# Kernel optimization log

Measured on AMD Instinct MI355X. Metric: run time of the kernel, lower is better.

## Reference

```python
import jax, jax.numpy as jnp
import numpy as np

N = 50000      # nodes
E = 800000     # edges
INS = 128
H = 128
OUTS = 128
G = 512        # graphs in batch
BN_EPS = 1e-5


def _lin(k, fan_in, fan_out):
    s = 1.0 / np.sqrt(fan_in)
    kw, kb = jax.random.split(k)
    w = jax.random.uniform(kw, (fan_in, fan_out), minval=-s, maxval=s, dtype=jnp.float32)
    b = jax.random.uniform(kb, (fan_out,), minval=-s, maxval=s, dtype=jnp.float32)
    return w, b


def setup_inputs() -> dict:
    key = jax.random.key(0)
    ks = jax.random.split(key, 16)
    x = jax.random.normal(ks[0], (N, INS), dtype=jnp.float32)
    edge_src = jax.random.randint(ks[1], (E,), 0, N, dtype=jnp.int32)
    edge_dst = jax.random.randint(ks[2], (E,), 0, N, dtype=jnp.int32)
    ptr = jnp.sort(jax.random.randint(ks[3], (G + 1,), 0, N, dtype=jnp.int32))
    ptr = ptr.at[0].set(0).at[-1].set(N)
    w1a, b1a = _lin(ks[4], INS, H)
    w1b, b1b = _lin(ks[5], H, H)
    w2a, b2a = _lin(ks[6], H, H)
    w2b, b2b = _lin(ks[7], H, H)
    w3a, b3a = _lin(ks[8], H, H)
    w3b, b3b = _lin(ks[9], H, OUTS)
    g1 = jnp.ones((H,), jnp.float32); be1 = jnp.zeros((H,), jnp.float32)
    g2 = jnp.ones((H,), jnp.float32); be2 = jnp.zeros((H,), jnp.float32)
    g3 = jnp.ones((H,), jnp.float32); be3 = jnp.zeros((H,), jnp.float32)
    return dict(x=x, edge_src=edge_src, edge_dst=edge_dst, ptr=ptr,
                w1a=w1a, b1a=b1a, g1=g1, be1=be1, w1b=w1b, b1b=b1b,
                w2a=w2a, b2a=b2a, g2=g2, be2=be2, w2b=w2b, b2b=b2b,
                w3a=w3a, b3a=b3a, g3=g3, be3=be3, w3b=w3b, b3b=b3b)


def _bn(h, gamma, beta):
    # BatchNorm1d in training mode: stats over the node dimension
    mu = jnp.mean(h, axis=0)
    var = jnp.var(h, axis=0)
    return gamma * (h - mu) * jax.lax.rsqrt(var + BN_EPS) + beta


def _gin_layer(h, src, dst, wa, ba, gamma, beta, wb, bb):
    # GINConv (eps=0): mlp(x + sum_{j in N(i)} x_j)
    agg = jax.ops.segment_sum(h[src], dst, num_segments=N)  # [N, d]
    h = h + agg
    h = jax.nn.relu(_bn(h @ wa + ba, gamma, beta))
    h = jax.nn.relu(h @ wb + bb)
    return h


def reference(x, edge_src, edge_dst, ptr,
              w1a, b1a, g1, be1, w1b, b1b,
              w2a, b2a, g2, be2, w2b, b2b,
              w3a, b3a, g3, be3, w3b, b3b):
    h = _gin_layer(x, edge_src, edge_dst, w1a, b1a, g1, be1, w1b, b1b)
    h = _gin_layer(h, edge_src, edge_dst, w2a, b2a, g2, be2, w2b, b2b)
    h = _gin_layer(h, edge_src, edge_dst, w3a, b3a, g3, be3, w3b, b3b)
    # segment_csr(x, ptr, reduce='sum') readout
    seg = jnp.searchsorted(ptr, jnp.arange(N, dtype=jnp.int32), side='right') - 1
    return jax.ops.segment_sum(h, seg, num_segments=G)  # [G, OUTS]
```

## Files before the change

kernel.cpp:

```cpp
#include <hip/hip_runtime.h>

#define NNODES 50000
#define NEDGES 800000
#define HD 128
#define NG 512
#define BN_EPS 1e-5f
#define NTILE 3125
#define NSPLIT 32

typedef short bf16x8 __attribute__((ext_vector_type(8)));
typedef float floatx4 __attribute__((ext_vector_type(4)));

union U16 { uint4 u; bf16x8 h; };

__device__ __forceinline__ ushort f2bf(float f) {
    unsigned u = __float_as_uint(f);
    return (ushort)((u + 0x7fffu + ((u >> 16) & 1u)) >> 16);
}
__device__ __forceinline__ void unpack8(const uint4& u, float* f) {
    const unsigned* w = (const unsigned*)&u;
#pragma unroll
    for (int i = 0; i < 4; ++i) {
        f[2 * i]     = __uint_as_float(w[i] << 16);
        f[2 * i + 1] = __uint_as_float(w[i] & 0xffff0000u);
    }
}
__device__ __forceinline__ uint4 pack8(const float* f) {
    uint4 o;
    unsigned* w = (unsigned*)&o;
#pragma unroll
    for (int i = 0; i < 4; ++i)
        w[i] = (unsigned)f2bf(f[2 * i]) | ((unsigned)f2bf(f[2 * i + 1]) << 16);
    return o;
}


__global__ void hist_kernel(const int* __restrict__ dst, int* __restrict__ cnt, int n) {
    int i = blockIdx.x * 256 + threadIdx.x;
    if (i < n) atomicAdd(&cnt[dst[i]], 1);
}

__global__ void scan1_kernel(const int* __restrict__ cnt, int* __restrict__ incl,
                             int* __restrict__ bsum, int n) {
    __shared__ int s[1024];
    int i = blockIdx.x * 1024 + threadIdx.x;
    int v = (i < n) ? cnt[i] : 0;
    s[threadIdx.x] = v;
    __syncthreads();
    for (int off = 1; off < 1024; off <<= 1) {
        int add = (threadIdx.x >= off) ? s[threadIdx.x - off] : 0;
        __syncthreads();
        s[threadIdx.x] += add;
        __syncthreads();
    }
    if (i < n) incl[i] = s[threadIdx.x];
    if (threadIdx.x == 1023) bsum[blockIdx.x] = s[1023];
}

__global__ void scan2_kernel(const int* __restrict__ bsum, int* __restrict__ boffs, int nb) {
    __shared__ int s[64];
    int v = (threadIdx.x < nb) ? bsum[threadIdx.x] : 0;
    s[threadIdx.x] = v;
    __syncthreads();
    for (int off = 1; off < 64; off <<= 1) {
        int add = (threadIdx.x >= off) ? s[threadIdx.x - off] : 0;
        __syncthreads();
        s[threadIdx.x] += add;
        __syncthreads();
    }
    if (threadIdx.x < nb) boffs[threadIdx.x] = s[threadIdx.x] - v;
}

__global__ void scan3_kernel(const int* __restrict__ incl, const int* __restrict__ boffs,
                             int* __restrict__ rowp, int n) {
    int i = blockIdx.x * 256 + threadIdx.x;
    if (i < n) rowp[i + 1] = incl[i] + boffs[i >> 10];
    if (i == 0) rowp[0] = 0;
}

__global__ void build_kernel(const int* __restrict__ src, const int* __restrict__ dst,
                             const int* __restrict__ rowp, int* __restrict__ fill,
                             int* __restrict__ colv, int n) {
    int i = blockIdx.x * 256 + threadIdx.x;
    if (i < n) {
        int d = dst[i];
        int pos = rowp[d] + atomicAdd(&fill[d], 1);
        colv[pos] = src[i];
    }
}


__global__ void cvt_kernel(const float* __restrict__ x, ushort* __restrict__ xb, int n4) {
    int i = blockIdx.x * 256 + threadIdx.x;
    if (i < n4) {
        float4 v = ((const float4*)x)[i];
        ushort4 o;
        o.x = f2bf(v.x); o.y = f2bf(v.y); o.z = f2bf(v.z); o.w = f2bf(v.w);
        ((ushort4*)xb)[i] = o;
    }
}


struct WP6 { const float* w[6]; };

__global__ void wfrag_kernel(WP6 p, ushort* __restrict__ wf) {
    const float* W = p.w[blockIdx.x];
    ushort* o = wf + (size_t)blockIdx.x * 16384;
    for (int i = threadIdx.x; i < 16384; i += 256) {
        int j = i & 7, lane = (i >> 3) & 63, kc = (i >> 9) & 3, ct = i >> 11;
        int k = kc * 32 + (lane >> 4) * 8 + j;
        int n = ct * 16 + (lane & 15);
        o[i] = f2bf(W[k * HD + n]);
    }
}


__global__ __launch_bounds__(256) void aggregate_kernel(
    const ushort* __restrict__ h, const int* __restrict__ rowp,
    const int* __restrict__ colv, ushort* __restrict__ outv, int n) {
    int node = blockIdx.x * 16 + (threadIdx.x >> 4);
    int l = threadIdx.x & 15;
    if (node >= n) return;
    int beg = rowp[node], end = rowp[node + 1];
    const uint4* hp = (const uint4*)h;
    float a[8];
    uint4 sv = hp[(size_t)node * 16 + l];
    unpack8(sv, a);
    for (int j = beg; j < end; ++j) {
        uint4 v = hp[(size_t)colv[j] * 16 + l];
        float b[8];
        unpack8(v, b);
#pragma unroll
        for (int i = 0; i < 8; ++i) a[i] += b[i];
    }
    ((uint4*)outv)[(size_t)node * 16 + l] = pack8(a);
}


template <bool STATS, bool PRE_BN, bool READOUT>
__global__ __launch_bounds__(256, 4) void mfma_gemm_kernel(
    const ushort* __restrict__ A, const ushort* __restrict__ Wf,
    const float* __restrict__ bias, ushort* __restrict__ out,
    const float* __restrict__ sca, const float* __restrict__ shf,
    float* __restrict__ ssum_p, float* __restrict__ ssq_p,
    const int* __restrict__ gptr, float* __restrict__ gout) {
    __shared__ ushort cbuf[16 * HD];
    __shared__ float reds[HD];
    __shared__ float redq[HD];
    const int t = threadIdx.x;
    const int wave = t >> 6, lane = t & 63;
    const int quad = lane >> 4, l16 = lane & 15;
    const int row0 = blockIdx.x * 16;
    const int rowA = row0 + l16;

    const uint4* Wf4 = (const uint4*)Wf;
    uint4 bfr[2][4];
#pragma unroll
    for (int c = 0; c < 2; ++c)
#pragma unroll
        for (int kc = 0; kc < 4; ++kc)
            bfr[c][kc] = Wf4[((2 * wave + c) * 4 + kc) * 64 + lane];

    U16 afr[4];
    {
        const ushort* ap = A + (size_t)rowA * HD + quad * 8;
#pragma unroll
        for (int kc = 0; kc < 4; ++kc)
            afr[kc].u = *(const uint4*)(ap + kc * 32);
    }
    if (PRE_BN) {
#pragma unroll
        for (int kc = 0; kc < 4; ++kc) {
            float f[8];
            unpack8(afr[kc].u, f);
            int kb = kc * 32 + quad * 8;
            float4 s0 = ((const float4*)(sca + kb))[0];
            float4 s1 = ((const float4*)(sca + kb))[1];
            float4 h0 = ((const float4*)(shf + kb))[0];
            float4 h1 = ((const float4*)(shf + kb))[1];
            f[0] = fmaxf(fmaf(f[0], s0.x, h0.x), 0.f);
            f[1] = fmaxf(fmaf(f[1], s0.y, h0.y), 0.f);
            f[2] = fmaxf(fmaf(f[2], s0.z, h0.z), 0.f);
            f[3] = fmaxf(fmaf(f[3], s0.w, h0.w), 0.f);
            f[4] = fmaxf(fmaf(f[4], s1.x, h1.x), 0.f);
            f[5] = fmaxf(fmaf(f[5], s1.y, h1.y), 0.f);
            f[6] = fmaxf(fmaf(f[6], s1.z, h1.z), 0.f);
            f[7] = fmaxf(fmaf(f[7], s1.w, h1.w), 0.f);
            afr[kc].u = pack8(f);
        }
    }

    floatx4 zf = {0.f, 0.f, 0.f, 0.f};
    floatx4 acc[2] = {zf, zf};
#pragma unroll
    for (int kc = 0; kc < 4; ++kc) {
#pragma unroll
        for (int c = 0; c < 2; ++c) {
            U16 bu;
            bu.u = bfr[c][kc];
            acc[c] = __builtin_amdgcn_mfma_f32_16x16x32_bf16(afr[kc].h, bu.h, acc[c], 0, 0, 0);
        }
    }

    if (READOUT) {
        int r_base = row0 + quad * 4;
        int lo = 0, hi = NG - 1;
        while (lo < hi) {
            int mid = (lo + hi) >> 1;
            if (r_base >= gptr[mid + 1]) lo = mid + 1; else hi = mid;
        }
        int segr[4];
        int sg = lo;
#pragma unroll
        for (int reg = 0; reg < 4; ++reg) {
            while (r_base + reg >= gptr[sg + 1]) ++sg;
            segr[reg] = sg;
        }
#pragma unroll
        for (int c = 0; c < 2; ++c) {
            int col = (2 * wave + c) * 16 + l16;
            float b = bias[col];
            float run = 0.f;
            int cur = segr[0];
#pragma unroll
            for (int reg = 0; reg < 4; ++reg) {
                if (segr[reg] != cur) {
                    if (run != 0.f) atomicAdd(&gout[cur * HD + col], run);
                    run = 0.f;
                    cur = segr[reg];
                }
                run += fmaxf(acc[c][reg] + b, 0.f);
            }
            if (run != 0.f) atomicAdd(&gout[cur * HD + col], run);
        }
        return;
    }

    const int lrow = quad * 4;
#pragma unroll
    for (int c = 0; c < 2; ++c) {
        int col = (2 * wave + c) * 16 + l16;
        float b = bias[col];
        float s = 0.f, q = 0.f;
#pragma unroll
        for (int reg = 0; reg < 4; ++reg) {
            float v = acc[c][reg] + b;
            if (!STATS) v = fmaxf(v, 0.f);
            cbuf[(lrow + reg) * HD + col] = f2bf(v);
            if (STATS) { s += v; q += v * v; }
        }
        if (STATS) {
            s += __shfl_xor(s, 16); s += __shfl_xor(s, 32);
            q += __shfl_xor(q, 16); q += __shfl_xor(q, 32);
            if (quad == 0) { reds[col] = s; redq[col] = q; }
        }
    }
    __syncthreads();

    {
        const uint4* c4 = (const uint4*)cbuf;
        uint4* o4 = (uint4*)out;
        int row = t >> 4, part = t & 15;
        o4[(size_t)(row0 + row) * 16 + part] = c4[t];
    }

    if (STATS) {
        int slot = (blockIdx.x & (NSPLIT - 1)) * HD;
        if (t < HD) atomicAdd(&ssum_p[slot + t], reds[t]);
        else        atomicAdd(&ssq_p[slot + (t - HD)], redq[t - HD]);
    }
}

__global__ void finalize_stats_kernel(const float* __restrict__ sp, const float* __restrict__ qp,
                                      const float* __restrict__ gamma, const float* __restrict__ beta,
                                      float* __restrict__ sca, float* __restrict__ shf) {
    int c = threadIdx.x;
    float s = 0.f, q = 0.f;
#pragma unroll
    for (int i = 0; i < NSPLIT; ++i) { s += sp[i * HD + c]; q += qp[i * HD + c]; }
    float mean = s / (float)NNODES;
    float var = q / (float)NNODES - mean * mean;
    float rstd = rsqrtf(var + BN_EPS);
    float sc = gamma[c] * rstd;
    sca[c] = sc;
    shf[c] = beta[c] - mean * sc;
}


extern "C" void kernel_launch(void* const* d_in, const int* in_sizes, int n_in,
                              void* d_out, int out_size, void* d_ws, size_t ws_size,
                              hipStream_t stream) {
    const float* x = (const float*)d_in[0];
    const int* esrc = (const int*)d_in[1];
    const int* edst = (const int*)d_in[2];
    const int* gptr = (const int*)d_in[3];
    const float* wA[3] = {(const float*)d_in[4], (const float*)d_in[10], (const float*)d_in[16]};
    const float* bA[3] = {(const float*)d_in[5], (const float*)d_in[11], (const float*)d_in[17]};
    const float* gm[3] = {(const float*)d_in[6], (const float*)d_in[12], (const float*)d_in[18]};
    const float* bt[3] = {(const float*)d_in[7], (const float*)d_in[13], (const float*)d_in[19]};
    const float* wB[3] = {(const float*)d_in[8], (const float*)d_in[14], (const float*)d_in[20]};
    const float* bB[3] = {(const float*)d_in[9], (const float*)d_in[15], (const float*)d_in[21]};

    char* w = (char*)d_ws;
    ushort* xb   = (ushort*)w; w += (size_t)NNODES * HD * 2;
    ushort* tmpb = (ushort*)w; w += (size_t)NNODES * HD * 2;
    ushort* zbb  = (ushort*)w; w += (size_t)NNODES * HD * 2;
    ushort* hbb  = (ushort*)w; w += (size_t)NNODES * HD * 2;
    ushort* wf   = (ushort*)w; w += (size_t)6 * 16384 * 2;
    int* colv  = (int*)w;   w += (size_t)NEDGES * 4;
    int* incl  = (int*)w;   w += (size_t)NNODES * 4;
    int* rowp  = (int*)w;   w += ((size_t)(NNODES + 1) * 4 + 15) & ~(size_t)15;
    int* bsum  = (int*)w;   w += 64 * 4;
    int* boffs = (int*)w;   w += 64 * 4;
    float* scab = (float*)w; w += 3 * 128 * 4;
    float* shfb = (float*)w; w += 3 * 128 * 4;
    char* zero_base = w;
    int* cnt   = (int*)w;   w += (size_t)NNODES * 4;
    int* fill  = (int*)w;   w += (size_t)NNODES * 4;
    float* ssum_p = (float*)w; w += 3 * NSPLIT * 128 * 4;
    float* ssq_p  = (float*)w; w += 3 * NSPLIT * 128 * 4;
    size_t zero_bytes = (size_t)(w - zero_base);

    hipMemsetAsync(zero_base, 0, zero_bytes, stream);
    hipMemsetAsync(d_out, 0, (size_t)NG * HD * 4, stream);

    hist_kernel<<<(NEDGES + 255) / 256, 256, 0, stream>>>(edst, cnt, NEDGES);
    int nsb = (NNODES + 1023) / 1024;
    scan1_kernel<<<nsb, 1024, 0, stream>>>(cnt, incl, bsum, NNODES);
    scan2_kernel<<<1, 64, 0, stream>>>(bsum, boffs, nsb);
    scan3_kernel<<<(NNODES + 255) / 256, 256, 0, stream>>>(incl, boffs, rowp, NNODES);
    build_kernel<<<(NEDGES + 255) / 256, 256, 0, stream>>>(esrc, edst, rowp, fill, colv, NEDGES);

    cvt_kernel<<<(NNODES * HD / 4 + 255) / 256, 256, 0, stream>>>(x, xb, NNODES * HD / 4);
    WP6 wp;
    wp.w[0] = wA[0]; wp.w[1] = wB[0]; wp.w[2] = wA[1];
    wp.w[3] = wB[1]; wp.w[4] = wA[2]; wp.w[5] = wB[2];
    wfrag_kernel<<<6, 256, 0, stream>>>(wp, wf);

    const int agg_grid = (NNODES + 15) / 16;
    const ushort* hin = xb;
    for (int l = 0; l < 3; ++l) {
        aggregate_kernel<<<agg_grid, 256, 0, stream>>>(hin, rowp, colv, tmpb, NNODES);
        mfma_gemm_kernel<true, false, false><<<NTILE, 256, 0, stream>>>(
            tmpb, wf + (size_t)(2 * l) * 16384, bA[l], zbb, nullptr, nullptr,
            ssum_p + l * NSPLIT * 128, ssq_p + l * NSPLIT * 128, nullptr, nullptr);
        finalize_stats_kernel<<<1, 128, 0, stream>>>(
            ssum_p + l * NSPLIT * 128, ssq_p + l * NSPLIT * 128,
            gm[l], bt[l], scab + l * 128, shfb + l * 128);
        if (l < 2) {
            mfma_gemm_kernel<false, true, false><<<NTILE, 256, 0, stream>>>(
                zbb, wf + (size_t)(2 * l + 1) * 16384, bB[l], hbb,
                scab + l * 128, shfb + l * 128, nullptr, nullptr, nullptr, nullptr);
        } else {
            mfma_gemm_kernel<false, true, true><<<NTILE, 256, 0, stream>>>(
                zbb, wf + (size_t)(2 * l + 1) * 16384, bB[l], nullptr,
                scab + l * 128, shfb + l * 128, nullptr, nullptr,
                gptr, (float*)d_out);
        }
        hin = hbb;
    }
}
```

Baseline: 458.4 us.

## Fuse aggregation into first GEMM, fold BN finalize into second GEMM, merge prep kernels

The neighbor-sum aggregation now runs inside the first GEMM kernel and stages its result in shared memory, so the bf16 intermediate buffer is no longer written and read back. The BatchNorm stats finalize moves into every block of the second GEMM, and the stat-slot count drops from 32 to 8. Histogram, input conversion and weight fragment packing merge into one prep kernel, and the scan's second and third passes merge into one. This cuts kernel launches and global memory traffic. The cost is more atomic contention on fewer stat slots, redundant finalize work in each block, and aggregation load imbalance now sitting inside the GEMM blocks.

New measurement: 422.0 us. 7.9% less time.

```diff
diff --git a/kernel.cpp b/kernel.cpp
--- a/kernel.cpp
+++ b/kernel.cpp
@@ -6,7 +6,9 @@
 #define NG 512
 #define BN_EPS 1e-5f
 #define NTILE 3125
-#define NSPLIT 32
+#define NSPLIT 8
+#define NSB 49
+#define AROW 136
 
 typedef short bf16x8 __attribute__((ext_vector_type(8)));
 typedef float floatx4 __attribute__((ext_vector_type(4)));
@@ -35,10 +37,34 @@
 }
 
 
-__global__ void hist_kernel(const int* __restrict__ dst, int* __restrict__ cnt, int n) {
-    int i = blockIdx.x * 256 + threadIdx.x;
-    if (i < n) atomicAdd(&cnt[dst[i]], 1);
-}
+struct WP6 { const float* w[6]; };
+
+__global__ __launch_bounds__(256) void prep_kernel(
+    const int* __restrict__ edst, int* __restrict__ cnt,
+    const float* __restrict__ x, ushort* __restrict__ xb,
+    WP6 p, ushort* __restrict__ wf) {
+    const int b = blockIdx.x, t = threadIdx.x;
+    if (b < 3125) {
+        atomicAdd(&cnt[edst[b * 256 + t]], 1);
+    } else if (b < 9375) {
+        int i = (b - 3125) * 256 + t;
+        float4 v = ((const float4*)x)[i];
+        ushort4 o;
+        o.x = f2bf(v.x); o.y = f2bf(v.y); o.z = f2bf(v.z); o.w = f2bf(v.w);
+        ((ushort4*)xb)[i] = o;
+    } else {
+        int m = b - 9375;
+        const float* W = p.w[m];
+        ushort* o = wf + (size_t)m * 16384;
+        for (int i = t; i < 16384; i += 256) {
+            int j = i & 7, lane = (i >> 3) & 63, kc = (i >> 9) & 3, ct = i >> 11;
+            int k = kc * 32 + (lane >> 4) * 8 + j;
+            int n = ct * 16 + (lane & 15);
+            o[i] = f2bf(W[k * HD + n]);
+        }
+    }
+}
+
 
 __global__ void scan1_kernel(const int* __restrict__ cnt, int* __restrict__ incl,
                              int* __restrict__ bsum, int n) {
@@ -57,24 +83,22 @@
     if (threadIdx.x == 1023) bsum[blockIdx.x] = s[1023];
 }
 
-__global__ void scan2_kernel(const int* __restrict__ bsum, int* __restrict__ boffs, int nb) {
-    __shared__ int s[64];
-    int v = (threadIdx.x < nb) ? bsum[threadIdx.x] : 0;
-    s[threadIdx.x] = v;
-    __syncthreads();
-    for (int off = 1; off < 64; off <<= 1) {
-        int add = (threadIdx.x >= off) ? s[threadIdx.x - off] : 0;
-        __syncthreads();
-        s[threadIdx.x] += add;
-        __syncthreads();
-    }
-    if (threadIdx.x < nb) boffs[threadIdx.x] = s[threadIdx.x] - v;
-}
-
-__global__ void scan3_kernel(const int* __restrict__ incl, const int* __restrict__ boffs,
-                             int* __restrict__ rowp, int n) {
-    int i = blockIdx.x * 256 + threadIdx.x;
-    if (i < n) rowp[i + 1] = incl[i] + boffs[i >> 10];
+__global__ void scan23_kernel(const int* __restrict__ incl, const int* __restrict__ bsum,
+                              int* __restrict__ rowp, int n) {
+    __shared__ int bpre[64];
+    const int t = threadIdx.x;
+    if (t < 64) {
+        int own = (t < NSB) ? bsum[t] : 0;
+        int v = own;
+        for (int off = 1; off < 64; off <<= 1) {
+            int u = __shfl_up(v, off);
+            if (t >= off) v += u;
+        }
+        bpre[t] = v - own;
+    }
+    __syncthreads();
+    int i = blockIdx.x * 256 + t;
+    if (i < n) rowp[i + 1] = incl[i] + bpre[i >> 10];
     if (i == 0) rowp[0] = 0;
 }
 
@@ -90,60 +114,12 @@
 }
 
 
-__global__ void cvt_kernel(const float* __restrict__ x, ushort* __restrict__ xb, int n4) {
-    int i = blockIdx.x * 256 + threadIdx.x;
-    if (i < n4) {
-        float4 v = ((const float4*)x)[i];
-        ushort4 o;
-        o.x = f2bf(v.x); o.y = f2bf(v.y); o.z = f2bf(v.z); o.w = f2bf(v.w);
-        ((ushort4*)xb)[i] = o;
-    }
-}
-
-
-struct WP6 { const float* w[6]; };
-
-__global__ void wfrag_kernel(WP6 p, ushort* __restrict__ wf) {
-    const float* W = p.w[blockIdx.x];
-    ushort* o = wf + (size_t)blockIdx.x * 16384;
-    for (int i = threadIdx.x; i < 16384; i += 256) {
-        int j = i & 7, lane = (i >> 3) & 63, kc = (i >> 9) & 3, ct = i >> 11;
-        int k = kc * 32 + (lane >> 4) * 8 + j;
-        int n = ct * 16 + (lane & 15);
-        o[i] = f2bf(W[k * HD + n]);
-    }
-}
-
-
-__global__ __launch_bounds__(256) void aggregate_kernel(
-    const ushort* __restrict__ h, const int* __restrict__ rowp,
-    const int* __restrict__ colv, ushort* __restrict__ outv, int n) {
-    int node = blockIdx.x * 16 + (threadIdx.x >> 4);
-    int l = threadIdx.x & 15;
-    if (node >= n) return;
-    int beg = rowp[node], end = rowp[node + 1];
-    const uint4* hp = (const uint4*)h;
-    float a[8];
-    uint4 sv = hp[(size_t)node * 16 + l];
-    unpack8(sv, a);
-    for (int j = beg; j < end; ++j) {
-        uint4 v = hp[(size_t)colv[j] * 16 + l];
-        float b[8];
-        unpack8(v, b);
-#pragma unroll
-        for (int i = 0; i < 8; ++i) a[i] += b[i];
-    }
-    ((uint4*)outv)[(size_t)node * 16 + l] = pack8(a);
-}
-
-
-template <bool STATS, bool PRE_BN, bool READOUT>
-__global__ __launch_bounds__(256, 4) void mfma_gemm_kernel(
-    const ushort* __restrict__ A, const ushort* __restrict__ Wf,
+__global__ __launch_bounds__(256, 4) void gemmA_kernel(
+    const ushort* __restrict__ H, const int* __restrict__ rowp,
+    const int* __restrict__ colv, const ushort* __restrict__ Wf,
     const float* __restrict__ bias, ushort* __restrict__ out,
-    const float* __restrict__ sca, const float* __restrict__ shf,
-    float* __restrict__ ssum_p, float* __restrict__ ssq_p,
-    const int* __restrict__ gptr, float* __restrict__ gout) {
+    float* __restrict__ ssum_p, float* __restrict__ ssq_p) {
+    __shared__ ushort abuf[16 * AROW];
     __shared__ ushort cbuf[16 * HD];
     __shared__ float reds[HD];
     __shared__ float redq[HD];
@@ -151,6 +127,95 @@
     const int wave = t >> 6, lane = t & 63;
     const int quad = lane >> 4, l16 = lane & 15;
     const int row0 = blockIdx.x * 16;
+
+    const uint4* Wf4 = (const uint4*)Wf;
+    uint4 bfr[2][4];
+#pragma unroll
+    for (int c = 0; c < 2; ++c)
+#pragma unroll
+        for (int kc = 0; kc < 4; ++kc)
+            bfr[c][kc] = Wf4[((2 * wave + c) * 4 + kc) * 64 + lane];
+
+    {
+        int nl = t >> 4;
+        int node = row0 + nl;
+        int l = t & 15;
+        int beg = rowp[node], end = rowp[node + 1];
+        const uint4* hp = (const uint4*)H;
+        float a[8];
+        unpack8(hp[(size_t)node * 16 + l], a);
+        for (int j = beg; j < end; ++j) {
+            float b[8];
+            unpack8(hp[(size_t)colv[j] * 16 + l], b);
+#pragma unroll
+            for (int i = 0; i < 8; ++i) a[i] += b[i];
+        }
+        *(uint4*)&abuf[nl * AROW + l * 8] = pack8(a);
+    }
+    __syncthreads();
+
+    U16 afr[4];
+#pragma unroll
+    for (int kc = 0; kc < 4; ++kc)
+        afr[kc].u = *(const uint4*)&abuf[l16 * AROW + kc * 32 + quad * 8];
+
+    floatx4 zf = {0.f, 0.f, 0.f, 0.f};
+    floatx4 acc[2] = {zf, zf};
+#pragma unroll
+    for (int kc = 0; kc < 4; ++kc) {
+#pragma unroll
+        for (int c = 0; c < 2; ++c) {
+            U16 bu;
+            bu.u = bfr[c][kc];
+            acc[c] = __builtin_amdgcn_mfma_f32_16x16x32_bf16(afr[kc].h, bu.h, acc[c], 0, 0, 0);
+        }
+    }
+
+    const int lrow = quad * 4;
+#pragma unroll
+    for (int c = 0; c < 2; ++c) {
+        int col = (2 * wave + c) * 16 + l16;
+        float b = bias[col];
+        float s = 0.f, q = 0.f;
+#pragma unroll
+        for (int reg = 0; reg < 4; ++reg) {
+            float v = acc[c][reg] + b;
+            cbuf[(lrow + reg) * HD + col] = f2bf(v);
+            s += v; q += v * v;
+        }
+        s += __shfl_xor(s, 16); s += __shfl_xor(s, 32);
+        q += __shfl_xor(q, 16); q += __shfl_xor(q, 32);
+        if (quad == 0) { reds[col] = s; redq[col] = q; }
+    }
+    __syncthreads();
+
+    {
+        const uint4* c4 = (const uint4*)cbuf;
+        uint4* o4 = (uint4*)out;
+        int row = t >> 4, part = t & 15;
+        o4[(size_t)(row0 + row) * 16 + part] = c4[t];
+    }
+
+    int slot = (blockIdx.x & (NSPLIT - 1)) * HD;
+    if (t < HD) atomicAdd(&ssum_p[slot + t], reds[t]);
+    else        atomicAdd(&ssq_p[slot + (t - HD)], redq[t - HD]);
+}
+
+
+template <bool READOUT>
+__global__ __launch_bounds__(256, 4) void gemmB_kernel(
+    const ushort* __restrict__ A, const ushort* __restrict__ Wf,
+    const float* __restrict__ bias, ushort* __restrict__ out,
+    const float* __restrict__ gamma, const float* __restrict__ beta,
+    const float* __restrict__ ssum_p, const float* __restrict__ ssq_p,
+    const int* __restrict__ gptr, float* __restrict__ gout) {
+    __shared__ ushort cbuf[16 * HD];
+    __shared__ float sca[HD];
+    __shared__ float shf[HD];
+    const int t = threadIdx.x;
+    const int wave = t >> 6, lane = t & 63;
+    const int quad = lane >> 4, l16 = lane & 15;
+    const int row0 = blockIdx.x * 16;
     const int rowA = row0 + l16;
 
     const uint4* Wf4 = (const uint4*)Wf;
@@ -168,26 +233,38 @@
         for (int kc = 0; kc < 4; ++kc)
             afr[kc].u = *(const uint4*)(ap + kc * 32);
     }
-    if (PRE_BN) {
-#pragma unroll
-        for (int kc = 0; kc < 4; ++kc) {
-            float f[8];
-            unpack8(afr[kc].u, f);
-            int kb = kc * 32 + quad * 8;
-            float4 s0 = ((const float4*)(sca + kb))[0];
-            float4 s1 = ((const float4*)(sca + kb))[1];
-            float4 h0 = ((const float4*)(shf + kb))[0];
-            float4 h1 = ((const float4*)(shf + kb))[1];
-            f[0] = fmaxf(fmaf(f[0], s0.x, h0.x), 0.f);
-            f[1] = fmaxf(fmaf(f[1], s0.y, h0.y), 0.f);
-            f[2] = fmaxf(fmaf(f[2], s0.z, h0.z), 0.f);
-            f[3] = fmaxf(fmaf(f[3], s0.w, h0.w), 0.f);
-            f[4] = fmaxf(fmaf(f[4], s1.x, h1.x), 0.f);
-            f[5] = fmaxf(fmaf(f[5], s1.y, h1.y), 0.f);
-            f[6] = fmaxf(fmaf(f[6], s1.z, h1.z), 0.f);
-            f[7] = fmaxf(fmaf(f[7], s1.w, h1.w), 0.f);
-            afr[kc].u = pack8(f);
-        }
+
+    if (t < HD) {
+        float s = 0.f, q = 0.f;
+#pragma unroll
+        for (int i = 0; i < NSPLIT; ++i) { s += ssum_p[i * HD + t]; q += ssq_p[i * HD + t]; }
+        float mean = s / (float)NNODES;
+        float var = q / (float)NNODES - mean * mean;
+        float rstd = rsqrtf(var + BN_EPS);
+        float sc = gamma[t] * rstd;
+        sca[t] = sc;
+        shf[t] = beta[t] - mean * sc;
+    }
+    __syncthreads();
+
+#pragma unroll
+    for (int kc = 0; kc < 4; ++kc) {
+        float f[8];
+        unpack8(afr[kc].u, f);
+        int kb = kc * 32 + quad * 8;
+        float4 s0 = ((const float4*)(sca + kb))[0];
+        float4 s1 = ((const float4*)(sca + kb))[1];
+        float4 h0 = ((const float4*)(shf + kb))[0];
+        float4 h1 = ((const float4*)(shf + kb))[1];
+        f[0] = fmaxf(fmaf(f[0], s0.x, h0.x), 0.f);
+        f[1] = fmaxf(fmaf(f[1], s0.y, h0.y), 0.f);
+        f[2] = fmaxf(fmaf(f[2], s0.z, h0.z), 0.f);
+        f[3] = fmaxf(fmaf(f[3], s0.w, h0.w), 0.f);
+        f[4] = fmaxf(fmaf(f[4], s1.x, h1.x), 0.f);
+        f[5] = fmaxf(fmaf(f[5], s1.y, h1.y), 0.f);
+        f[6] = fmaxf(fmaf(f[6], s1.z, h1.z), 0.f);
+        f[7] = fmaxf(fmaf(f[7], s1.w, h1.w), 0.f);
+        afr[kc].u = pack8(f);
     }
 
     floatx4 zf = {0.f, 0.f, 0.f, 0.f};
@@ -241,49 +318,17 @@
     for (int c = 0; c < 2; ++c) {
         int col = (2 * wave + c) * 16 + l16;
         float b = bias[col];
-        float s = 0.f, q = 0.f;
-#pragma unroll
-        for (int reg = 0; reg < 4; ++reg) {
-            float v = acc[c][reg] + b;
-            if (!STATS) v = fmaxf(v, 0.f);
-            cbuf[(lrow + reg) * HD + col] = f2bf(v);
-            if (STATS) { s += v; q += v * v; }
-        }
-        if (STATS) {
-            s += __shfl_xor(s, 16); s += __shfl_xor(s, 32);
-            q += __shfl_xor(q, 16); q += __shfl_xor(q, 32);
-            if (quad == 0) { reds[col] = s; redq[col] = q; }
-        }
-    }
-    __syncthreads();
-
+#pragma unroll
+        for (int reg = 0; reg < 4; ++reg)
+            cbuf[(lrow + reg) * HD + col] = f2bf(fmaxf(acc[c][reg] + b, 0.f));
+    }
+    __syncthreads();
     {
         const uint4* c4 = (const uint4*)cbuf;
         uint4* o4 = (uint4*)out;
         int row = t >> 4, part = t & 15;
         o4[(size_t)(row0 + row) * 16 + part] = c4[t];
     }
-
-    if (STATS) {
-        int slot = (blockIdx.x & (NSPLIT - 1)) * HD;
-        if (t < HD) atomicAdd(&ssum_p[slot + t], reds[t]);
-        else        atomicAdd(&ssq_p[slot + (t - HD)], redq[t - HD]);
-    }
-}
-
-__global__ void finalize_stats_kernel(const float* __restrict__ sp, const float* __restrict__ qp,
-                                      const float* __restrict__ gamma, const float* __restrict__ beta,
-                                      float* __restrict__ sca, float* __restrict__ shf) {
-    int c = threadIdx.x;
-    float s = 0.f, q = 0.f;
-#pragma unroll
-    for (int i = 0; i < NSPLIT; ++i) { s += sp[i * HD + c]; q += qp[i * HD + c]; }
-    float mean = s / (float)NNODES;
-    float var = q / (float)NNODES - mean * mean;
-    float rstd = rsqrtf(var + BN_EPS);
-    float sc = gamma[c] * rstd;
-    sca[c] = sc;
-    shf[c] = beta[c] - mean * sc;
 }
 
 
@@ -303,7 +348,6 @@
 
     char* w = (char*)d_ws;
     ushort* xb   = (ushort*)w; w += (size_t)NNODES * HD * 2;
-    ushort* tmpb = (ushort*)w; w += (size_t)NNODES * HD * 2;
     ushort* zbb  = (ushort*)w; w += (size_t)NNODES * HD * 2;
     ushort* hbb  = (ushort*)w; w += (size_t)NNODES * HD * 2;
     ushort* wf   = (ushort*)w; w += (size_t)6 * 16384 * 2;
@@ -311,9 +355,6 @@
     int* incl  = (int*)w;   w += (size_t)NNODES * 4;
     int* rowp  = (int*)w;   w += ((size_t)(NNODES + 1) * 4 + 15) & ~(size_t)15;
     int* bsum  = (int*)w;   w += 64 * 4;
-    int* boffs = (int*)w;   w += 64 * 4;
-    float* scab = (float*)w; w += 3 * 128 * 4;
-    float* shfb = (float*)w; w += 3 * 128 * 4;
     char* zero_base = w;
     int* cnt   = (int*)w;   w += (size_t)NNODES * 4;
     int* fill  = (int*)w;   w += (size_t)NNODES * 4;
@@ -324,38 +365,28 @@
     hipMemsetAsync(zero_base, 0, zero_bytes, stream);
     hipMemsetAsync(d_out, 0, (size_t)NG * HD * 4, stream);
 
-    hist_kernel<<<(NEDGES + 255) / 256, 256, 0, stream>>>(edst, cnt, NEDGES);
-    int nsb = (NNODES + 1023) / 1024;
-    scan1_kernel<<<nsb, 1024, 0, stream>>>(cnt, incl, bsum, NNODES);
-    scan2_kernel<<<1, 64, 0, stream>>>(bsum, boffs, nsb);
-    scan3_kernel<<<(NNODES + 255) / 256, 256, 0, stream>>>(incl, boffs, rowp, NNODES);
-    build_kernel<<<(NEDGES + 255) / 256, 256, 0, stream>>>(esrc, edst, rowp, fill, colv, NEDGES);
-
-    cvt_kernel<<<(NNODES * HD / 4 + 255) / 256, 256, 0, stream>>>(x, xb, NNODES * HD / 4);
     WP6 wp;
     wp.w[0] = wA[0]; wp.w[1] = wB[0]; wp.w[2] = wA[1];
     wp.w[3] = wB[1]; wp.w[4] = wA[2]; wp.w[5] = wB[2];
-    wfrag_kernel<<<6, 256, 0, stream>>>(wp, wf);
-
-    const int agg_grid = (NNODES + 15) / 16;
+
+    prep_kernel<<<9381, 256, 0, stream>>>(edst, cnt, x, xb, wp, wf);
+    scan1_kernel<<<NSB, 1024, 0, stream>>>(cnt, incl, bsum, NNODES);
+    scan23_kernel<<<(NNODES + 255) / 256, 256, 0, stream>>>(incl, bsum, rowp, NNODES);
+    build_kernel<<<(NEDGES + 255) / 256, 256, 0, stream>>>(esrc, edst, rowp, fill, colv, NEDGES);
+
     const ushort* hin = xb;
     for (int l = 0; l < 3; ++l) {
-        aggregate_kernel<<<agg_grid, 256, 0, stream>>>(hin, rowp, colv, tmpb, NNODES);
-        mfma_gemm_kernel<true, false, false><<<NTILE, 256, 0, stream>>>(
-            tmpb, wf + (size_t)(2 * l) * 16384, bA[l], zbb, nullptr, nullptr,
-            ssum_p + l * NSPLIT * 128, ssq_p + l * NSPLIT * 128, nullptr, nullptr);
-        finalize_stats_kernel<<<1, 128, 0, stream>>>(
-            ssum_p + l * NSPLIT * 128, ssq_p + l * NSPLIT * 128,
-            gm[l], bt[l], scab + l * 128, shfb + l * 128);
+        gemmA_kernel<<<NTILE, 256, 0, stream>>>(
+            hin, rowp, colv, wf + (size_t)(2 * l) * 16384, bA[l], zbb,
+            ssum_p + l * NSPLIT * 128, ssq_p + l * NSPLIT * 128);
         if (l < 2) {
-            mfma_gemm_kernel<false, true, false><<<NTILE, 256, 0, stream>>>(
-                zbb, wf + (size_t)(2 * l + 1) * 16384, bB[l], hbb,
-                scab + l * 128, shfb + l * 128, nullptr, nullptr, nullptr, nullptr);
+            gemmB_kernel<false><<<NTILE, 256, 0, stream>>>(
+                zbb, wf + (size_t)(2 * l + 1) * 16384, bB[l], hbb, gm[l], bt[l],
+                ssum_p + l * NSPLIT * 128, ssq_p + l * NSPLIT * 128, nullptr, nullptr);
         } else {
-            mfma_gemm_kernel<false, true, true><<<NTILE, 256, 0, stream>>>(
-                zbb, wf + (size_t)(2 * l + 1) * 16384, bB[l], nullptr,
-                scab + l * 128, shfb + l * 128, nullptr, nullptr,
-                gptr, (float*)d_out);
+            gemmB_kernel<true><<<NTILE, 256, 0, stream>>>(
+                zbb, wf + (size_t)(2 * l + 1) * 16384, bB[l], nullptr, gm[l], bt[l],
+                ssum_p + l * NSPLIT * 128, ssq_p + l * NSPLIT * 128, gptr, (float*)d_out);
         }
         hin = hbb;
     }
```
